# Kernel optimization log

Measured on AMD Instinct MI355X. Metric: run time of the kernel, lower is better.

## Reference

```python
import jax, jax.numpy as jnp
import numpy as np

S = 16        # neighbor samples per layer
NL = 2        # number of GNN layers


def setup_inputs() -> dict:
    key = jax.random.key(0)
    ks = jax.random.split(key, 12)
    N_NODES, D, E, NMP, DEG, N_EDGE, B, NC = 50000, 128, 32, 3, 32, 200000, 1024, 8
    sc = 0.05
    return {
        "ids": jax.random.randint(ks[0], (B,), 0, N_NODES, dtype=jnp.int32),
        "feats": jax.random.normal(ks[1], (N_NODES, D), jnp.float32),
        "edge_emb": jax.random.normal(ks[2], (NMP, N_EDGE, E), jnp.float32),
        "adj_nodes": jax.random.randint(ks[3], (NMP, N_NODES, DEG), 0, N_NODES, dtype=jnp.int32),
        "adj_edges": jax.random.randint(ks[4], (NMP, N_NODES, DEG), 0, N_EDGE, dtype=jnp.int32),
        "W_self": jax.random.normal(ks[5], (NMP, NL, D, D), jnp.float32) * sc,
        "W_neigh": jax.random.normal(ks[6], (NMP, NL, D + E, D), jnp.float32) * sc,
        "W_edge": jax.random.normal(ks[7], (NMP, NL, 2 * D + E, E), jnp.float32) * sc,
        "attn": jax.random.normal(ks[8], (D,), jnp.float32) * sc,
        "fc_w": jax.random.normal(ks[9], (D, NC), jnp.float32) * sc,
        "fc_b": jnp.zeros((NC,), jnp.float32),
    }


def reference(ids, feats, edge_emb, adj_nodes, adj_edges, W_self, W_neigh, W_edge, attn, fc_w, fc_b):
    NMP = adj_nodes.shape[0]
    outs = []
    for mp in range(NMP):
        # --- sample neighbor tree (deterministic: first S columns) ---
        cur = ids
        all_feats = [feats[cur]]
        all_edges = []
        for _ in range(NL):
            nb = adj_nodes[mp][cur][:, :S].reshape(-1)     # [N*S]
            eid = adj_edges[mp][cur][:, :S].reshape(-1)    # [N*S]
            all_edges.append(edge_emb[mp][eid])            # [N*S, E]
            cur = nb
            all_feats.append(feats[cur])
        # --- per-layer aggregation + edge update ---
        for l in range(NL):
            new_feats = []
            for k in range(len(all_feats) - 1):
                xs, xn, ee = all_feats[k], all_feats[k + 1], all_edges[k]
                N = xs.shape[0]
                # mean over sampled neighbors of [neigh_feat || edge_emb]
                nin = jnp.concatenate(
                    [xn.reshape(N, S, -1), ee.reshape(N, S, -1)], axis=-1
                ).mean(axis=1)                             # [N, D+E]
                new_feats.append(jax.nn.relu(xs @ W_self[mp, l] + nin @ W_neigh[mp, l]))
            all_feats = new_feats  # dropout is identity in eval mode
            new_edges = []
            for k in range(len(all_edges) - 1):
                xs, xn, ee = all_feats[k], all_feats[k + 1], all_edges[k]
                rep = jnp.repeat(xs, S, axis=0)            # [N*S, D]
                new_edges.append(jax.nn.relu(
                    jnp.concatenate([rep, xn, ee], axis=-1) @ W_edge[mp, l]))
            all_edges = new_edges
        outs.append(all_feats[0])                          # [B, D]
    stacked = jnp.stack(outs)                              # [NMP, B, D]
    # metapath attention fuse
    scores = jnp.tanh(jnp.einsum('mbd,d->mb', stacked, attn))
    beta = jax.nn.softmax(scores, axis=0)
    emb = jnp.einsum('mb,mbd->bd', beta, stacked)          # [B, D]
    # F.normalize(dim=1)
    emb = emb / jnp.maximum(jnp.linalg.norm(emb, axis=1, keepdims=True), 1e-12)
    return emb @ fc_w + fc_b
```

## Files before the change

### kernel.cpp

```cpp
#include <hip/hip_runtime.h>

#define NNODES  50000
#define D       128
#define E       32
#define NMP     3
#define DEG     32
#define NEDGE   200000
#define B       1024
#define NC      8
#define S       16

#define RPM      17408
#define NKT      9
#define WSTRIDE  36864
#define WESTRIDE 9216

#define CONV_TASKS (1600000 + 6 * WSTRIDE + 3 * WESTRIDE)
#define TOT_TASKS  (CONV_TASKS + 3 * RPM)

typedef float f4 __attribute__((ext_vector_type(4)));
typedef short bh8 __attribute__((ext_vector_type(8)));
typedef unsigned int uv4 __attribute__((ext_vector_type(4)));
typedef unsigned int uv2 __attribute__((ext_vector_type(2)));
typedef int iv4 __attribute__((ext_vector_type(4)));
typedef int iv2 __attribute__((ext_vector_type(2)));

static __device__ __forceinline__ unsigned short f2bf(float f) {
    unsigned int u = __float_as_uint(f);
    u = u + 0x7FFFu + ((u >> 16) & 1u);
    return (unsigned short)(u >> 16);
}
static __device__ __forceinline__ float bf2f(unsigned short h) {
    return __uint_as_float(((unsigned int)h) << 16);
}

__global__ __launch_bounds__(256) void convsamp_k(
    const float* __restrict__ feats, const float* __restrict__ Ws,
    const float* __restrict__ Wn, const float* __restrict__ We,
    const int* __restrict__ ids, const int* __restrict__ adjn,
    const int* __restrict__ adje,
    unsigned short* __restrict__ fb, unsigned short* __restrict__ WT0,
    unsigned short* __restrict__ WTe, int* __restrict__ gx, int* __restrict__ eid1)
{
    int i = blockIdx.x * 256 + threadIdx.x;
    if (i < 1600000) {
        float4 v = ((const float4*)feats)[i];
        unsigned int p0 = (unsigned int)f2bf(v.x) | ((unsigned int)f2bf(v.y) << 16);
        unsigned int p1 = (unsigned int)f2bf(v.z) | ((unsigned int)f2bf(v.w) << 16);
        ((uint2*)fb)[i] = make_uint2(p0, p1);
    } else if (i < 1600000 + 6 * WSTRIDE) {
        int i2 = i - 1600000;
        int ml = i2 / WSTRIDE, e = i2 % WSTRIDE;
        int j = e & 7, t1 = e >> 3;
        int n = t1 & 127, t2 = t1 >> 7;
        int q = t2 & 3, kt = t2 >> 2;
        int k = kt * 32 + q * 8 + j;
        float v = (k < 128) ? Ws[((size_t)ml * 128 + k) * 128 + n]
                            : Wn[((size_t)ml * 160 + (k - 128)) * 128 + n];
        WT0[(size_t)ml * WSTRIDE + e] = f2bf(v);
    } else if (i < CONV_TASKS) {
        int i3 = i - 1600000 - 6 * WSTRIDE;
        int mp = i3 / WESTRIDE, e = i3 % WESTRIDE;
        int j = e & 7, t1 = e >> 3;
        int n = t1 & 31, t2 = t1 >> 5;
        int q = t2 & 3, kt = t2 >> 2;
        int k = kt * 32 + q * 8 + j;
        float v = We[(((size_t)mp * 2) * 288 + k) * 32 + n];
        WTe[(size_t)mp * WESTRIDE + e] = f2bf(v);
    } else if (i < TOT_TASKS) {
        int i4 = i - CONV_TASKS;
        int mp = i4 / RPM, r = i4 % RPM;
        if (r < 16384) {
            int node = ids[r >> 4];
            gx[mp * RPM + r]     = adjn[((size_t)mp * NNODES + node) * DEG + (r & 15)];
            eid1[mp * 16384 + r] = adje[((size_t)mp * NNODES + node) * DEG + (r & 15)];
        } else {
            gx[mp * RPM + r] = ids[r - 16384];
        }
    }
}

__global__ __launch_bounds__(256, 4) void aggfeat_k(
    const unsigned short* __restrict__ fb, const float* __restrict__ edge_emb,
    const int* __restrict__ adjn, const int* __restrict__ adje,
    const int* __restrict__ gx, const int* __restrict__ eid1,
    const unsigned short* __restrict__ WT0,
    unsigned short* __restrict__ fout)
{
    __shared__ unsigned short Asm[16][136];
    __shared__ unsigned short Nsm[16][168];
    const int mp = blockIdx.y;
    const int w = threadIdx.x >> 6, l = threadIdx.x & 63;
    const int r0 = blockIdx.x * 16;
    const unsigned int* fb32 = (const unsigned int*)fb;
    const float* ee = edge_emb + (size_t)mp * NEDGE * E;
    const float inv = 1.0f / (float)S;
    const int g = l >> 4, c = l & 15;
    const int d8 = l & 7;

    int srcs[4];
#pragma unroll
    for (int rr = 0; rr < 4; ++rr)
        srcs[rr] = gx[mp * RPM + r0 + w * 4 + rr];

    iv4 nIdx[4]; iv2 eIdx[4]; unsigned int selfu[4];
#pragma unroll
    for (int rr = 0; rr < 4; ++rr) {
        const int* nb = adjn + ((size_t)mp * NNODES + srcs[rr]) * DEG;
        const int* eb = adje + ((size_t)mp * NNODES + srcs[rr]) * DEG;
        nIdx[rr] = *(const iv4*)(nb + 4 * g);
        eIdx[rr] = *(const iv2*)(eb + 2 * (l >> 3));
        selfu[rr] = fb32[(size_t)srcs[rr] * 64 + l];
    }

#pragma unroll
    for (int pp = 0; pp < 2; ++pp) {
        const int lra = w * 4 + 2 * pp, lrb = lra + 1;
        const int ia = 2 * pp, ib = 2 * pp + 1;

        uv4 gA[4], gB[4];
#pragma unroll
        for (int p = 0; p < 4; ++p)
            gA[p] = *(const uv4*)(fb32 + (size_t)nIdx[ia][p] * 64 + c * 4);
#pragma unroll
        for (int p = 0; p < 4; ++p)
            gB[p] = *(const uv4*)(fb32 + (size_t)nIdx[ib][p] * 64 + c * 4);
        f4 eA0 = *(const f4*)(ee + (size_t)eIdx[ia][0] * E + d8 * 4);
        f4 eA1 = *(const f4*)(ee + (size_t)eIdx[ia][1] * E + d8 * 4);
        f4 eB0 = *(const f4*)(ee + (size_t)eIdx[ib][0] * E + d8 * 4);
        f4 eB1 = *(const f4*)(ee + (size_t)eIdx[ib][1] * E + d8 * 4);

        float accA[8], accB[8];
#pragma unroll
        for (int d = 0; d < 8; ++d) { accA[d] = 0.f; accB[d] = 0.f; }
#pragma unroll
        for (int p = 0; p < 4; ++p)
#pragma unroll
            for (int qq = 0; qq < 4; ++qq) {
                unsigned int ua = gA[p][qq], ub = gB[p][qq];
                accA[2 * qq]     += __uint_as_float(ua << 16);
                accA[2 * qq + 1] += __uint_as_float(ua & 0xffff0000u);
                accB[2 * qq]     += __uint_as_float(ub << 16);
                accB[2 * qq + 1] += __uint_as_float(ub & 0xffff0000u);
            }
#pragma unroll
        for (int d = 0; d < 8; ++d) {
            accA[d] += __shfl_xor(accA[d], 16);
            accA[d] += __shfl_xor(accA[d], 32);
            accB[d] += __shfl_xor(accB[d], 16);
            accB[d] += __shfl_xor(accB[d], 32);
        }
        float feA[4], feB[4];
#pragma unroll
        for (int qq = 0; qq < 4; ++qq) {
            feA[qq] = eA0[qq] + eA1[qq];
            feB[qq] = eB0[qq] + eB1[qq];
            feA[qq] += __shfl_xor(feA[qq], 8);
            feA[qq] += __shfl_xor(feA[qq], 16);
            feA[qq] += __shfl_xor(feA[qq], 32);
            feB[qq] += __shfl_xor(feB[qq], 8);
            feB[qq] += __shfl_xor(feB[qq], 16);
            feB[qq] += __shfl_xor(feB[qq], 32);
        }

        ((unsigned int*)&Asm[lra][0])[l] = selfu[ia];
        ((unsigned int*)&Asm[lrb][0])[l] = selfu[ib];
        if (g == 0) {
            uv4 oa, ob;
#pragma unroll
            for (int qq = 0; qq < 4; ++qq) {
                oa[qq] = (unsigned int)f2bf(accA[2 * qq] * inv)
                       | ((unsigned int)f2bf(accA[2 * qq + 1] * inv) << 16);
                ob[qq] = (unsigned int)f2bf(accB[2 * qq] * inv)
                       | ((unsigned int)f2bf(accB[2 * qq + 1] * inv) << 16);
            }
            *(uv4*)&Nsm[lra][c * 8] = oa;
            *(uv4*)&Nsm[lrb][c * 8] = ob;
        }
        if (l < 8) {
            uv2 oa, ob;
            oa[0] = (unsigned int)f2bf(feA[0] * inv) | ((unsigned int)f2bf(feA[1] * inv) << 16);
            oa[1] = (unsigned int)f2bf(feA[2] * inv) | ((unsigned int)f2bf(feA[3] * inv) << 16);
            ob[0] = (unsigned int)f2bf(feB[0] * inv) | ((unsigned int)f2bf(feB[1] * inv) << 16);
            ob[1] = (unsigned int)f2bf(feB[2] * inv) | ((unsigned int)f2bf(feB[3] * inv) << 16);
            *(uv2*)&Nsm[lra][128 + d8 * 4] = oa;
            *(uv2*)&Nsm[lrb][128 + d8 * 4] = ob;
        }
    }
    __syncthreads();

    const int q = l >> 4, lm = l & 15;
    const unsigned short* wb = WT0 + (size_t)mp * 2 * WSTRIDE;

    f4 acc[2];
    acc[0] = (f4){0.f, 0.f, 0.f, 0.f};
    acc[1] = (f4){0.f, 0.f, 0.f, 0.f};

#pragma unroll
    for (int kt = 0; kt < NKT; ++kt) {
        const int k0 = kt * 32 + q * 8;
        bh8 a = (k0 < 128) ? *(const bh8*)&Asm[lm][k0]
                           : *(const bh8*)&Nsm[lm][k0 - 128];
        const unsigned short* wrow = wb + ((size_t)(kt * 4 + q) * 128 + lm) * 8;
#pragma unroll
        for (int ntl = 0; ntl < 2; ++ntl) {
            bh8 bf = *(const bh8*)(wrow + (w * 2 + ntl) * 16 * 8);
            acc[ntl] = __builtin_amdgcn_mfma_f32_16x16x32_bf16(a, bf, acc[ntl], 0, 0, 0);
        }
    }

#pragma unroll
    for (int ntl = 0; ntl < 2; ++ntl)
#pragma unroll
        for (int rr = 0; rr < 4; ++rr) {
            int row = r0 + q * 4 + rr;
            int col = (w * 2 + ntl) * 16 + lm;
            fout[((size_t)mp * RPM + row) * 128 + col] = f2bf(fmaxf(acc[ntl][rr], 0.f));
        }
}

__global__ __launch_bounds__(256) void edgeagg_k(
    const unsigned short* __restrict__ fout, const float* __restrict__ edge_emb,
    const int* __restrict__ eid1, const unsigned short* __restrict__ WTe,
    unsigned short* __restrict__ agg1)
{
    const int mp = blockIdx.y;
    const int w = threadIdx.x >> 6, l = threadIdx.x & 63;
    const int q = l >> 4, lm = l & 15;
    const int m0 = blockIdx.x * 64 + w * 16;
    const unsigned short* we = WTe + (size_t)mp * WESTRIDE;
    const unsigned short* f1base = fout + (size_t)mp * RPM * 128;
    const unsigned short* f0base = fout + ((size_t)mp * RPM + 16384) * 128;
    const float* ee = edge_emb + (size_t)mp * NEDGE * E;
    const float inv = 1.0f / (float)S;

    const int row = m0 + lm;
    const unsigned short* a1p = f1base + (size_t)row * 128;
    const unsigned short* a0p = f0base + (size_t)(row >> 4) * 128;
    const int eidL = eid1[mp * 16384 + row];

    f4 acc[2];
    acc[0] = (f4){0.f, 0.f, 0.f, 0.f};
    acc[1] = (f4){0.f, 0.f, 0.f, 0.f};

#pragma unroll
    for (int kt = 0; kt < NKT; ++kt) {
        const int k0 = kt * 32 + q * 8;
        bh8 a;
        if (kt < 4) {
            a = *(const bh8*)(a0p + k0);
        } else if (kt < 8) {
            a = *(const bh8*)(a1p + (k0 - 128));
        } else {
            const float* ep = ee + (size_t)eidL * E + q * 8;
            float4 v0 = *(const float4*)ep;
            float4 v1 = *(const float4*)(ep + 4);
            bh8 tv;
            tv[0] = (short)f2bf(v0.x); tv[1] = (short)f2bf(v0.y);
            tv[2] = (short)f2bf(v0.z); tv[3] = (short)f2bf(v0.w);
            tv[4] = (short)f2bf(v1.x); tv[5] = (short)f2bf(v1.y);
            tv[6] = (short)f2bf(v1.z); tv[7] = (short)f2bf(v1.w);
            a = tv;
        }
        const unsigned short* wrow = we + ((size_t)(kt * 4 + q) * 32 + lm) * 8;
        bh8 b0 = *(const bh8*)(wrow);
        bh8 b1 = *(const bh8*)(wrow + 16 * 8);
        acc[0] = __builtin_amdgcn_mfma_f32_16x16x32_bf16(a, b0, acc[0], 0, 0, 0);
        acc[1] = __builtin_amdgcn_mfma_f32_16x16x32_bf16(a, b1, acc[1], 0, 0, 0);
    }

    const int seg = m0 >> 4;
#pragma unroll
    for (int nt = 0; nt < 2; ++nt) {
        float ps = 0.f;
#pragma unroll
        for (int rr = 0; rr < 4; ++rr) ps += fmaxf(acc[nt][rr], 0.f);
        ps += __shfl_xor(ps, 16);
        ps += __shfl_xor(ps, 32);
        if (l < 16)
            agg1[((size_t)mp * B + seg) * 160 + 128 + nt * 16 + lm] = f2bf(ps * inv);
    }

    {
        const unsigned short* fr = f1base + (size_t)seg * 16 * 128;
        float s0 = 0.f, s1 = 0.f;
#pragma unroll
        for (int j = 0; j < S; ++j) {
            unsigned int u = ((const unsigned int*)(fr + j * 128))[l];
            s0 += bf2f((unsigned short)(u & 0xFFFF));
            s1 += bf2f((unsigned short)(u >> 16));
        }
        ((unsigned int*)(agg1 + ((size_t)mp * B + seg) * 160))[l] =
            (unsigned int)f2bf(s0 * inv) | ((unsigned int)f2bf(s1 * inv) << 16);
    }
}

__global__ __launch_bounds__(256) void feat1fin_k(
    const unsigned short* __restrict__ fout, const unsigned short* __restrict__ agg1,
    const unsigned short* __restrict__ WT0,
    const float* __restrict__ attn, const float* __restrict__ fcw,
    const float* __restrict__ fcb, float* __restrict__ out)
{
    __shared__ float sbuf[NMP][16][132];
    const int w = threadIdx.x >> 6, l = threadIdx.x & 63;
    const int q = l >> 4, lm = l & 15;
    const int m0 = blockIdx.x * 16;

    for (int task = w; task < 6; task += 4) {
        const int mp = task >> 1, nh = task & 1;
        const int row = m0 + lm;
        const unsigned short* ap = fout + ((size_t)mp * RPM + 16384 + row) * 128;
        const unsigned short* np = agg1 + ((size_t)mp * B + row) * 160;
        const unsigned short* wb = WT0 + ((size_t)mp * 2 + 1) * WSTRIDE;

        f4 acc[4];
#pragma unroll
        for (int nt = 0; nt < 4; ++nt) acc[nt] = (f4){0.f, 0.f, 0.f, 0.f};
#pragma unroll
        for (int kt = 0; kt < NKT; ++kt) {
            const int k0 = kt * 32 + q * 8;
            bh8 a = (k0 < 128) ? *(const bh8*)(ap + k0) : *(const bh8*)(np + (k0 - 128));
            const unsigned short* wrow = wb + ((size_t)(kt * 4 + q) * 128 + lm) * 8;
#pragma unroll
            for (int nt = 0; nt < 4; ++nt) {
                bh8 bf = *(const bh8*)(wrow + (nh * 4 + nt) * 16 * 8);
                acc[nt] = __builtin_amdgcn_mfma_f32_16x16x32_bf16(a, bf, acc[nt], 0, 0, 0);
            }
        }
#pragma unroll
        for (int nt = 0; nt < 4; ++nt)
#pragma unroll
            for (int rr = 0; rr < 4; ++rr)
                sbuf[mp][q * 4 + rr][(nh * 4 + nt) * 16 + lm] = fmaxf(acc[nt][rr], 0.f);
    }
    __syncthreads();

    if (threadIdx.x < 128) {
        const int row = threadIdx.x >> 3;
        const int j = threadIdx.x & 7;
        const int d0 = j * 16;
        float sc[NMP];
#pragma unroll
        for (int mp = 0; mp < NMP; ++mp) {
            float p = 0.f;
#pragma unroll
            for (int d = 0; d < 16; ++d) p += sbuf[mp][row][d0 + d] * attn[d0 + d];
            p += __shfl_xor(p, 1); p += __shfl_xor(p, 2); p += __shfl_xor(p, 4);
            sc[mp] = tanhf(p);
        }
        float mx = fmaxf(sc[0], fmaxf(sc[1], sc[2]));
        float e0 = expf(sc[0] - mx), e1 = expf(sc[1] - mx), e2 = expf(sc[2] - mx);
        float isum = 1.f / (e0 + e1 + e2);
        float b0 = e0 * isum, b1 = e1 * isum, b2 = e2 * isum;

        float emb[16];
        float nn = 0.f;
#pragma unroll
        for (int d = 0; d < 16; ++d) {
            float v = b0 * sbuf[0][row][d0 + d] + b1 * sbuf[1][row][d0 + d]
                    + b2 * sbuf[2][row][d0 + d];
            emb[d] = v;
            nn += v * v;
        }
        nn += __shfl_xor(nn, 1); nn += __shfl_xor(nn, 2); nn += __shfl_xor(nn, 4);
        float innorm = 1.f / fmaxf(sqrtf(nn), 1e-12f);
#pragma unroll
        for (int d = 0; d < 16; ++d) emb[d] *= innorm;

#pragma unroll
        for (int cc = 0; cc < NC; ++cc) {
            float p = 0.f;
#pragma unroll
            for (int d = 0; d < 16; ++d) p += emb[d] * fcw[(d0 + d) * NC + cc];
            p += __shfl_xor(p, 1); p += __shfl_xor(p, 2); p += __shfl_xor(p, 4);
            if (j == cc) out[(size_t)(m0 + row) * NC + cc] = p + fcb[cc];
        }
    }
}

extern "C" void kernel_launch(void* const* d_in, const int* in_sizes, int n_in,
                              void* d_out, int out_size, void* d_ws, size_t ws_size,
                              hipStream_t stream) {
    const int* ids        = (const int*)d_in[0];
    const float* feats    = (const float*)d_in[1];
    const float* edge_emb = (const float*)d_in[2];
    const int* adjn       = (const int*)d_in[3];
    const int* adje       = (const int*)d_in[4];
    const float* Ws       = (const float*)d_in[5];
    const float* Wn       = (const float*)d_in[6];
    const float* We       = (const float*)d_in[7];
    const float* attn     = (const float*)d_in[8];
    const float* fcw      = (const float*)d_in[9];
    const float* fcb      = (const float*)d_in[10];
    float* out = (float*)d_out;

    char* p = (char*)d_ws;
    unsigned short* WT0 = (unsigned short*)p; p += (size_t)6 * WSTRIDE * 2;
    unsigned short* WTe = (unsigned short*)p; p += (size_t)3 * WESTRIDE * 2;
    unsigned short* fb  = (unsigned short*)p; p += (size_t)NNODES * 128 * 2;
    int* gx   = (int*)p;                      p += (size_t)3 * RPM * 4;
    int* eid1 = (int*)p;                      p += (size_t)3 * 16384 * 4;
    unsigned short* fout = (unsigned short*)p; p += (size_t)3 * RPM * 128 * 2;
    unsigned short* agg1 = (unsigned short*)p; p += (size_t)3 * B * 160 * 2;

    convsamp_k<<<TOT_TASKS / 256, 256, 0, stream>>>(feats, Ws, Wn, We, ids, adjn, adje,
                                                    fb, WT0, WTe, gx, eid1);
    aggfeat_k<<<dim3(RPM / 16, 3), 256, 0, stream>>>(fb, edge_emb, adjn, adje, gx, eid1,
                                                     WT0, fout);
    edgeagg_k<<<dim3(256, 3), 256, 0, stream>>>(fout, edge_emb, eid1, WTe, agg1);
    feat1fin_k<<<64, 256, 0, stream>>>(fout, agg1, WT0, attn, fcw, fcb, out);
}
```

Baseline: 225.5 us.

## Batch all neighbor gathers up front and fuse layer-1 root GEMM into edge kernel

Result: no change. 224.8 us (-0.3%).

```diff
diff --git a/kernel.cpp b/kernel.cpp
--- a/kernel.cpp
+++ b/kernel.cpp
@@ -80,7 +80,7 @@
     }
 }
 
-__global__ __launch_bounds__(256, 4) void aggfeat_k(
+__global__ __launch_bounds__(256, 3) void aggfeat_k(
     const unsigned short* __restrict__ fb, const float* __restrict__ edge_emb,
     const int* __restrict__ adjn, const int* __restrict__ adje,
     const int* __restrict__ gx, const int* __restrict__ eid1,
@@ -98,93 +98,71 @@
     const int g = l >> 4, c = l & 15;
     const int d8 = l & 7;
 
-    int srcs[4];
-#pragma unroll
-    for (int rr = 0; rr < 4; ++rr)
-        srcs[rr] = gx[mp * RPM + r0 + w * 4 + rr];
+    iv4 srcv = *(const iv4*)(gx + mp * RPM + r0 + w * 4);
 
     iv4 nIdx[4]; iv2 eIdx[4]; unsigned int selfu[4];
 #pragma unroll
     for (int rr = 0; rr < 4; ++rr) {
-        const int* nb = adjn + ((size_t)mp * NNODES + srcs[rr]) * DEG;
-        const int* eb = adje + ((size_t)mp * NNODES + srcs[rr]) * DEG;
-        nIdx[rr] = *(const iv4*)(nb + 4 * g);
-        eIdx[rr] = *(const iv2*)(eb + 2 * (l >> 3));
-        selfu[rr] = fb32[(size_t)srcs[rr] * 64 + l];
-    }
-
-#pragma unroll
-    for (int pp = 0; pp < 2; ++pp) {
-        const int lra = w * 4 + 2 * pp, lrb = lra + 1;
-        const int ia = 2 * pp, ib = 2 * pp + 1;
-
-        uv4 gA[4], gB[4];
+        const int src = srcv[rr];
+        nIdx[rr]  = *(const iv4*)(adjn + ((size_t)mp * NNODES + src) * DEG + 4 * g);
+        eIdx[rr]  = *(const iv2*)(adje + ((size_t)mp * NNODES + src) * DEG + 2 * (l >> 3));
+        selfu[rr] = fb32[(size_t)src * 64 + l];
+    }
+
+    uv4 gN[4][4];
+    f4  gE[4][2];
+#pragma unroll
+    for (int rr = 0; rr < 4; ++rr) {
 #pragma unroll
         for (int p = 0; p < 4; ++p)
-            gA[p] = *(const uv4*)(fb32 + (size_t)nIdx[ia][p] * 64 + c * 4);
+            gN[rr][p] = *(const uv4*)(fb32 + (size_t)nIdx[rr][p] * 64 + c * 4);
+        gE[rr][0] = *(const f4*)(ee + (size_t)eIdx[rr][0] * E + d8 * 4);
+        gE[rr][1] = *(const f4*)(ee + (size_t)eIdx[rr][1] * E + d8 * 4);
+    }
+    asm volatile("" ::: "memory");
+
+#pragma unroll
+    for (int rr = 0; rr < 4; ++rr) {
+        const int lr = w * 4 + rr;
+        float acc[8];
+#pragma unroll
+        for (int d = 0; d < 8; ++d) acc[d] = 0.f;
 #pragma unroll
         for (int p = 0; p < 4; ++p)
-            gB[p] = *(const uv4*)(fb32 + (size_t)nIdx[ib][p] * 64 + c * 4);
-        f4 eA0 = *(const f4*)(ee + (size_t)eIdx[ia][0] * E + d8 * 4);
-        f4 eA1 = *(const f4*)(ee + (size_t)eIdx[ia][1] * E + d8 * 4);
-        f4 eB0 = *(const f4*)(ee + (size_t)eIdx[ib][0] * E + d8 * 4);
-        f4 eB1 = *(const f4*)(ee + (size_t)eIdx[ib][1] * E + d8 * 4);
-
-        float accA[8], accB[8];
-#pragma unroll
-        for (int d = 0; d < 8; ++d) { accA[d] = 0.f; accB[d] = 0.f; }
-#pragma unroll
-        for (int p = 0; p < 4; ++p)
 #pragma unroll
             for (int qq = 0; qq < 4; ++qq) {
-                unsigned int ua = gA[p][qq], ub = gB[p][qq];
-                accA[2 * qq]     += __uint_as_float(ua << 16);
-                accA[2 * qq + 1] += __uint_as_float(ua & 0xffff0000u);
-                accB[2 * qq]     += __uint_as_float(ub << 16);
-                accB[2 * qq + 1] += __uint_as_float(ub & 0xffff0000u);
+                unsigned int u = gN[rr][p][qq];
+                acc[2 * qq]     += __uint_as_float(u << 16);
+                acc[2 * qq + 1] += __uint_as_float(u & 0xffff0000u);
             }
 #pragma unroll
         for (int d = 0; d < 8; ++d) {
-            accA[d] += __shfl_xor(accA[d], 16);
-            accA[d] += __shfl_xor(accA[d], 32);
-            accB[d] += __shfl_xor(accB[d], 16);
-            accB[d] += __shfl_xor(accB[d], 32);
-        }
-        float feA[4], feB[4];
+            acc[d] += __shfl_xor(acc[d], 16);
+            acc[d] += __shfl_xor(acc[d], 32);
+        }
+        float fe[4];
 #pragma unroll
         for (int qq = 0; qq < 4; ++qq) {
-            feA[qq] = eA0[qq] + eA1[qq];
-            feB[qq] = eB0[qq] + eB1[qq];
-            feA[qq] += __shfl_xor(feA[qq], 8);
-            feA[qq] += __shfl_xor(feA[qq], 16);
-            feA[qq] += __shfl_xor(feA[qq], 32);
-            feB[qq] += __shfl_xor(feB[qq], 8);
-            feB[qq] += __shfl_xor(feB[qq], 16);
-            feB[qq] += __shfl_xor(feB[qq], 32);
-        }
-
-        ((unsigned int*)&Asm[lra][0])[l] = selfu[ia];
-        ((unsigned int*)&Asm[lrb][0])[l] = selfu[ib];
+            fe[qq] = gE[rr][0][qq] + gE[rr][1][qq];
+            fe[qq] += __shfl_xor(fe[qq], 8);
+            fe[qq] += __shfl_xor(fe[qq], 16);
+            fe[qq] += __shfl_xor(fe[qq], 32);
+        }
+
+        ((unsigned int*)&Asm[lr][0])[l] = selfu[rr];
         if (g == 0) {
-            uv4 oa, ob;
-#pragma unroll
-            for (int qq = 0; qq < 4; ++qq) {
-                oa[qq] = (unsigned int)f2bf(accA[2 * qq] * inv)
-                       | ((unsigned int)f2bf(accA[2 * qq + 1] * inv) << 16);
-                ob[qq] = (unsigned int)f2bf(accB[2 * qq] * inv)
-                       | ((unsigned int)f2bf(accB[2 * qq + 1] * inv) << 16);
-            }
-            *(uv4*)&Nsm[lra][c * 8] = oa;
-            *(uv4*)&Nsm[lrb][c * 8] = ob;
+            uv4 o;
+#pragma unroll
+            for (int qq = 0; qq < 4; ++qq)
+                o[qq] = (unsigned int)f2bf(acc[2 * qq] * inv)
+                      | ((unsigned int)f2bf(acc[2 * qq + 1] * inv) << 16);
+            *(uv4*)&Nsm[lr][c * 8] = o;
         }
         if (l < 8) {
-            uv2 oa, ob;
-            oa[0] = (unsigned int)f2bf(feA[0] * inv) | ((unsigned int)f2bf(feA[1] * inv) << 16);
-            oa[1] = (unsigned int)f2bf(feA[2] * inv) | ((unsigned int)f2bf(feA[3] * inv) << 16);
-            ob[0] = (unsigned int)f2bf(feB[0] * inv) | ((unsigned int)f2bf(feB[1] * inv) << 16);
-            ob[1] = (unsigned int)f2bf(feB[2] * inv) | ((unsigned int)f2bf(feB[3] * inv) << 16);
-            *(uv2*)&Nsm[lra][128 + d8 * 4] = oa;
-            *(uv2*)&Nsm[lrb][128 + d8 * 4] = ob;
+            uv2 o;
+            o[0] = (unsigned int)f2bf(fe[0] * inv) | ((unsigned int)f2bf(fe[1] * inv) << 16);
+            o[1] = (unsigned int)f2bf(fe[2] * inv) | ((unsigned int)f2bf(fe[3] * inv) << 16);
+            *(uv2*)&Nsm[lr][128 + d8 * 4] = o;
         }
     }
     __syncthreads();
@@ -222,8 +200,10 @@
 __global__ __launch_bounds__(256) void edgeagg_k(
     const unsigned short* __restrict__ fout, const float* __restrict__ edge_emb,
     const int* __restrict__ eid1, const unsigned short* __restrict__ WTe,
-    unsigned short* __restrict__ agg1)
+    const unsigned short* __restrict__ WT0,
+    float* __restrict__ femb)
 {
+    __shared__ unsigned short As2[4][304];
     const int mp = blockIdx.y;
     const int w = threadIdx.x >> 6, l = threadIdx.x & 63;
     const int q = l >> 4, lm = l & 15;
@@ -269,7 +249,6 @@
         acc[1] = __builtin_amdgcn_mfma_f32_16x16x32_bf16(a, b1, acc[1], 0, 0, 0);
     }
 
-    const int seg = m0 >> 4;
 #pragma unroll
     for (int nt = 0; nt < 2; ++nt) {
         float ps = 0.f;
@@ -278,10 +257,14 @@
         ps += __shfl_xor(ps, 16);
         ps += __shfl_xor(ps, 32);
         if (l < 16)
-            agg1[((size_t)mp * B + seg) * 160 + 128 + nt * 16 + lm] = f2bf(ps * inv);
+            As2[w][256 + nt * 16 + lm] = f2bf(ps * inv);
     }
 
     {
+        const int seg = m0 >> 4;
+        unsigned int f0u = ((const unsigned int*)a0p)[l];
+        ((unsigned int*)&As2[w][0])[l] = f0u;
+
         const unsigned short* fr = f1base + (size_t)seg * 16 * 128;
         float s0 = 0.f, s1 = 0.f;
 #pragma unroll
@@ -290,91 +273,92 @@
             s0 += bf2f((unsigned short)(u & 0xFFFF));
             s1 += bf2f((unsigned short)(u >> 16));
         }
-        ((unsigned int*)(agg1 + ((size_t)mp * B + seg) * 160))[l] =
+        ((unsigned int*)&As2[w][0])[64 + l] =
             (unsigned int)f2bf(s0 * inv) | ((unsigned int)f2bf(s1 * inv) << 16);
     }
-}
-
-__global__ __launch_bounds__(256) void feat1fin_k(
-    const unsigned short* __restrict__ fout, const unsigned short* __restrict__ agg1,
-    const unsigned short* __restrict__ WT0,
-    const float* __restrict__ attn, const float* __restrict__ fcw,
-    const float* __restrict__ fcb, float* __restrict__ out)
+    __syncthreads();
+
+    const unsigned short* wb1 = WT0 + ((size_t)mp * 2 + 1) * WSTRIDE;
+    f4 acc2[2];
+    acc2[0] = (f4){0.f, 0.f, 0.f, 0.f};
+    acc2[1] = (f4){0.f, 0.f, 0.f, 0.f};
+
+#pragma unroll
+    for (int kt = 0; kt < NKT; ++kt) {
+        const int k0 = kt * 32 + q * 8;
+        bh8 a;
+        if (lm < 4) a = *(const bh8*)&As2[lm][k0];
+        else        a = (bh8){0, 0, 0, 0, 0, 0, 0, 0};
+        const unsigned short* wrow = wb1 + ((size_t)(kt * 4 + q) * 128 + lm) * 8;
+#pragma unroll
+        for (int ntl = 0; ntl < 2; ++ntl) {
+            bh8 bf = *(const bh8*)(wrow + (w * 2 + ntl) * 16 * 8);
+            acc2[ntl] = __builtin_amdgcn_mfma_f32_16x16x32_bf16(a, bf, acc2[ntl], 0, 0, 0);
+        }
+    }
+    if (q == 0) {
+#pragma unroll
+        for (int ntl = 0; ntl < 2; ++ntl)
+#pragma unroll
+            for (int rr = 0; rr < 4; ++rr) {
+                int seg = blockIdx.x * 4 + rr;
+                femb[((size_t)mp * B + seg) * 128 + (w * 2 + ntl) * 16 + lm] =
+                    fmaxf(acc2[ntl][rr], 0.f);
+            }
+    }
+}
+
+__global__ __launch_bounds__(256) void fin_k(
+    const float* __restrict__ femb, const float* __restrict__ attn,
+    const float* __restrict__ fcw, const float* __restrict__ fcb,
+    float* __restrict__ out)
 {
-    __shared__ float sbuf[NMP][16][132];
-    const int w = threadIdx.x >> 6, l = threadIdx.x & 63;
-    const int q = l >> 4, lm = l & 15;
-    const int m0 = blockIdx.x * 16;
-
-    for (int task = w; task < 6; task += 4) {
-        const int mp = task >> 1, nh = task & 1;
-        const int row = m0 + lm;
-        const unsigned short* ap = fout + ((size_t)mp * RPM + 16384 + row) * 128;
-        const unsigned short* np = agg1 + ((size_t)mp * B + row) * 160;
-        const unsigned short* wb = WT0 + ((size_t)mp * 2 + 1) * WSTRIDE;
-
-        f4 acc[4];
-#pragma unroll
-        for (int nt = 0; nt < 4; ++nt) acc[nt] = (f4){0.f, 0.f, 0.f, 0.f};
-#pragma unroll
-        for (int kt = 0; kt < NKT; ++kt) {
-            const int k0 = kt * 32 + q * 8;
-            bh8 a = (k0 < 128) ? *(const bh8*)(ap + k0) : *(const bh8*)(np + (k0 - 128));
-            const unsigned short* wrow = wb + ((size_t)(kt * 4 + q) * 128 + lm) * 8;
-#pragma unroll
-            for (int nt = 0; nt < 4; ++nt) {
-                bh8 bf = *(const bh8*)(wrow + (nh * 4 + nt) * 16 * 8);
-                acc[nt] = __builtin_amdgcn_mfma_f32_16x16x32_bf16(a, bf, acc[nt], 0, 0, 0);
-            }
-        }
-#pragma unroll
-        for (int nt = 0; nt < 4; ++nt)
-#pragma unroll
-            for (int rr = 0; rr < 4; ++rr)
-                sbuf[mp][q * 4 + rr][(nh * 4 + nt) * 16 + lm] = fmaxf(acc[nt][rr], 0.f);
-    }
-    __syncthreads();
-
-    if (threadIdx.x < 128) {
-        const int row = threadIdx.x >> 3;
-        const int j = threadIdx.x & 7;
-        const int d0 = j * 16;
-        float sc[NMP];
-#pragma unroll
-        for (int mp = 0; mp < NMP; ++mp) {
-            float p = 0.f;
-#pragma unroll
-            for (int d = 0; d < 16; ++d) p += sbuf[mp][row][d0 + d] * attn[d0 + d];
-            p += __shfl_xor(p, 1); p += __shfl_xor(p, 2); p += __shfl_xor(p, 4);
-            sc[mp] = tanhf(p);
-        }
-        float mx = fmaxf(sc[0], fmaxf(sc[1], sc[2]));
-        float e0 = expf(sc[0] - mx), e1 = expf(sc[1] - mx), e2 = expf(sc[2] - mx);
-        float isum = 1.f / (e0 + e1 + e2);
-        float b0 = e0 * isum, b1 = e1 * isum, b2 = e2 * isum;
-
-        float emb[16];
-        float nn = 0.f;
-#pragma unroll
-        for (int d = 0; d < 16; ++d) {
-            float v = b0 * sbuf[0][row][d0 + d] + b1 * sbuf[1][row][d0 + d]
-                    + b2 * sbuf[2][row][d0 + d];
-            emb[d] = v;
-            nn += v * v;
-        }
-        nn += __shfl_xor(nn, 1); nn += __shfl_xor(nn, 2); nn += __shfl_xor(nn, 4);
-        float innorm = 1.f / fmaxf(sqrtf(nn), 1e-12f);
-#pragma unroll
-        for (int d = 0; d < 16; ++d) emb[d] *= innorm;
-
-#pragma unroll
-        for (int cc = 0; cc < NC; ++cc) {
-            float p = 0.f;
-#pragma unroll
-            for (int d = 0; d < 16; ++d) p += emb[d] * fcw[(d0 + d) * NC + cc];
-            p += __shfl_xor(p, 1); p += __shfl_xor(p, 2); p += __shfl_xor(p, 4);
-            if (j == cc) out[(size_t)(m0 + row) * NC + cc] = p + fcb[cc];
-        }
+    const int row = blockIdx.x * 32 + (threadIdx.x >> 3);
+    const int j = threadIdx.x & 7;
+    const int d0 = j * 16;
+
+    float v[NMP][16];
+#pragma unroll
+    for (int mp = 0; mp < NMP; ++mp)
+#pragma unroll
+        for (int t = 0; t < 4; ++t)
+            *(f4*)&v[mp][t * 4] =
+                *(const f4*)&femb[((size_t)mp * B + row) * 128 + d0 + t * 4];
+
+    float sc[NMP];
+#pragma unroll
+    for (int mp = 0; mp < NMP; ++mp) {
+        float p = 0.f;
+#pragma unroll
+        for (int d = 0; d < 16; ++d) p += v[mp][d] * attn[d0 + d];
+        p += __shfl_xor(p, 1); p += __shfl_xor(p, 2); p += __shfl_xor(p, 4);
+        sc[mp] = tanhf(p);
+    }
+    float mx = fmaxf(sc[0], fmaxf(sc[1], sc[2]));
+    float e0 = expf(sc[0] - mx), e1 = expf(sc[1] - mx), e2 = expf(sc[2] - mx);
+    float isum = 1.f / (e0 + e1 + e2);
+    float b0 = e0 * isum, b1 = e1 * isum, b2 = e2 * isum;
+
+    float emb[16];
+    float nn = 0.f;
+#pragma unroll
+    for (int d = 0; d < 16; ++d) {
+        float vv = b0 * v[0][d] + b1 * v[1][d] + b2 * v[2][d];
+        emb[d] = vv;
+        nn += vv * vv;
+    }
+    nn += __shfl_xor(nn, 1); nn += __shfl_xor(nn, 2); nn += __shfl_xor(nn, 4);
+    float innorm = 1.f / fmaxf(sqrtf(nn), 1e-12f);
+#pragma unroll
+    for (int d = 0; d < 16; ++d) emb[d] *= innorm;
+
+#pragma unroll
+    for (int cc = 0; cc < NC; ++cc) {
+        float p = 0.f;
+#pragma unroll
+        for (int d = 0; d < 16; ++d) p += emb[d] * fcw[(d0 + d) * NC + cc];
+        p += __shfl_xor(p, 1); p += __shfl_xor(p, 2); p += __shfl_xor(p, 4);
+        if (j == cc) out[(size_t)row * NC + cc] = p + fcb[cc];
     }
 }
 
@@ -401,12 +385,12 @@
     int* gx   = (int*)p;                      p += (size_t)3 * RPM * 4;
     int* eid1 = (int*)p;                      p += (size_t)3 * 16384 * 4;
     unsigned short* fout = (unsigned short*)p; p += (size_t)3 * RPM * 128 * 2;
-    unsigned short* agg1 = (unsigned short*)p; p += (size_t)3 * B * 160 * 2;
+    float* femb = (float*)p;                   p += (size_t)3 * B * 128 * 4;
 
     convsamp_k<<<TOT_TASKS / 256, 256, 0, stream>>>(feats, Ws, Wn, We, ids, adjn, adje,
                                                     fb, WT0, WTe, gx, eid1);
     aggfeat_k<<<dim3(RPM / 16, 3), 256, 0, stream>>>(fb, edge_emb, adjn, adje, gx, eid1,
                                                      WT0, fout);
-    edgeagg_k<<<dim3(256, 3), 256, 0, stream>>>(fout, edge_emb, eid1, WTe, agg1);
-    feat1fin_k<<<64, 256, 0, stream>>>(fout, agg1, WT0, attn, fcw, fcb, out);
-}
+    edgeagg_k<<<dim3(256, 3), 256, 0, stream>>>(fout, edge_emb, eid1, WTe, WT0, femb);
+    fin_k<<<32, 256, 0, stream>>>(femb, attn, fcw, fcb, out);
+}
```
